# Kernel tuning notes

Hardware: AMD Instinct MI355X
Metric: run time of the kernel (lower is better)

The kernel has to match this reference:

```python
import jax, jax.numpy as jnp
import numpy as np

FEAT_DIM = 128

def conv3(x, w, b):
    y = jax.lax.conv_general_dilated(x, w, (1, 1), 'SAME', dimension_numbers=('NCHW', 'OIHW', 'NCHW'))
    return y + b[None, :, None, None]

def edsr(x, hw, hb, rw, rb, tw, tb):
    # EDSR baseline encoder (no upsampling): head conv, n resblocks, tail conv, global skip
    x = conv3(x, hw, hb)
    res = x
    for i in range(rw.shape[0]):
        t = jax.nn.relu(conv3(res, rw[i, 0], rb[i, 0]))
        res = res + conv3(t, rw[i, 1], rb[i, 1])
    return conv3(res, tw, tb) + x

def maxpool(x, k):
    return jax.lax.reduce_window(x, -jnp.inf, jax.lax.max, (1, 1, k, k), (1, 1, k, k), 'VALID')

def make_coord(h, w):
    ys = -1.0 + (2.0 * jnp.arange(h, dtype=jnp.float32) + 1.0) / h
    xs = -1.0 + (2.0 * jnp.arange(w, dtype=jnp.float32) + 1.0) / w
    yy, xx = jnp.meshgrid(ys, xs, indexing='ij')
    return jnp.stack([yy, xx], axis=-1)  # [h,w,2] (y,x)

def sample_nearest(img, coord):
    # F.grid_sample nearest, align_corners=False, zeros padding.
    # img [b,c,hi,wi]; coord [b,N,2] normalized (y,x) -> [b,N,c]
    b, c, hi, wi = img.shape
    iy = jnp.round(((coord[..., 0] + 1.0) * hi - 1.0) / 2.0)
    ix = jnp.round(((coord[..., 1] + 1.0) * wi - 1.0) / 2.0)
    valid = (iy >= 0) & (iy < hi) & (ix >= 0) & (ix < wi)
    idx = (jnp.clip(iy, 0, hi - 1) * wi + jnp.clip(ix, 0, wi - 1)).astype(jnp.int32)
    out = jnp.take_along_axis(img.reshape(b, c, hi * wi), idx[:, None, :], axis=2)
    out = jnp.where(valid[:, None, :], out, jnp.zeros((), img.dtype))
    return out.transpose(0, 2, 1)

def mlp2(x, w1, b1, w2, b2):
    return jax.nn.gelu(x @ w1 + b1, approximate=False) @ w2 + b2

def level(feat, coord, hr_guide, hr_guide_lr, im_w, im_b, wg, ffn, residual):
    b, c, h, w = feat.shape
    Hh, Ww = hr_guide.shape[2], hr_guide.shape[3]
    N = coord.shape[0]
    coord = jnp.broadcast_to(coord[None], (b, N, 2))
    fc = jnp.broadcast_to(make_coord(h, w).transpose(2, 0, 1)[None], (b, 2, h, w))
    g_s = sample_nearest(hr_guide, coord)  # [b,N,guide_dim]
    scale = jnp.array([h, w], dtype=jnp.float32)
    preds = []
    for vx in (-1.0, 1.0):
        for vy in (-1.0, 1.0):
            coord_ = coord + jnp.array([vx / h, vy / w], dtype=jnp.float32)
            f_s = sample_nearest(feat, coord_)
            gl_s = sample_nearest(hr_guide_lr, coord_)
            c_s = sample_nearest(fc, coord_)
            rel = (coord - c_s) * scale
            inp = jnp.concatenate([f_s, g_s, gl_s, rel], axis=-1)  # [b,N,3*fd+2]
            pred = jax.nn.relu(inp @ im_w + im_b)  # MLP(hidden_list=None): Linear+ReLU
            preds.append(pred[..., :FEAT_DIM])
            preds.append(pred[..., FEAT_DIM:])
    preds = jnp.stack(preds, axis=-2)  # [b,N,8,fd]
    weight = jax.nn.softmax(mlp2(preds, *wg), axis=-2)
    recon = jnp.sum(preds * weight, axis=-2)  # [b,N,fd]
    out = mlp2(recon, *ffn)
    if residual:
        out = out + recon
    return out.transpose(0, 2, 1).reshape(b, -1, Hh, Ww)

def setup_inputs():
    ks = jax.random.split(jax.random.key(0), 24)
    fd, nb, nsb = 128, 31, 3
    B, H, W, hlr = 16, 64, 64, 16
    def w_(k, shape, fan):
        return jax.random.normal(k, shape, dtype=jnp.float32) * (fan ** -0.5)
    return {
        'HR_MSI': jax.random.normal(ks[0], (B, nsb, H, W), dtype=jnp.float32),
        'lms': jax.random.normal(ks[1], (B, nb, H, W), dtype=jnp.float32),
        'LR_HSI': jax.random.normal(ks[2], (B, nb, hlr, hlr), dtype=jnp.float32),
        'spa_head_w': w_(ks[3], (fd, nsb + nb, 3, 3), (nsb + nb) * 9), 'spa_head_b': jnp.zeros((fd,)),
        'spa_res_w': w_(ks[4], (4, 2, fd, fd, 3, 3), fd * 9), 'spa_res_b': jnp.zeros((4, 2, fd)),
        'spa_tail_w': w_(ks[5], (fd, fd, 3, 3), fd * 9), 'spa_tail_b': jnp.zeros((fd,)),
        'spe_head_w': w_(ks[6], (fd, nb, 3, 3), nb * 9), 'spe_head_b': jnp.zeros((fd,)),
        'spe_res_w': w_(ks[7], (4, 2, fd, fd, 3, 3), fd * 9), 'spe_res_b': jnp.zeros((4, 2, fd)),
        'spe_tail_w': w_(ks[8], (fd, fd, 3, 3), fd * 9), 'spe_tail_b': jnp.zeros((fd,)),
        'l1_w': w_(ks[9], (fd * 3 + 2, fd * 2), fd * 3 + 2), 'l1_b': jnp.zeros((fd * 2,)),
        'wg32_w1': w_(ks[10], (fd, 64), fd), 'wg32_b1': jnp.zeros((64,)),
        'wg32_w2': w_(ks[11], (64, fd), 64), 'wg32_b2': jnp.zeros((fd,)),
        'ffn32_w1': w_(ks[12], (fd, 64), fd), 'ffn32_b1': jnp.zeros((64,)),
        'ffn32_w2': w_(ks[13], (64, fd), 64), 'ffn32_b2': jnp.zeros((fd,)),
        'l2_w': w_(ks[14], (fd * 3 + 2, fd * 2), fd * 3 + 2), 'l2_b': jnp.zeros((fd * 2,)),
        'wg64_w1': w_(ks[15], (fd, 64), fd), 'wg64_b1': jnp.zeros((64,)),
        'wg64_w2': w_(ks[16], (64, fd), 64), 'wg64_b2': jnp.zeros((fd,)),
        'ffn64_w1': w_(ks[17], (fd, 64), fd), 'ffn64_b1': jnp.zeros((64,)),
        'ffn64_w2': w_(ks[18], (64, nb), 64), 'ffn64_b2': jnp.zeros((nb,)),
    }

def reference(HR_MSI, lms, LR_HSI, spa_head_w, spa_head_b, spa_res_w, spa_res_b, spa_tail_w, spa_tail_b, spe_head_w, spe_head_b, spe_res_w, spe_res_b, spe_tail_w, spe_tail_b, l1_w, l1_b, wg32_w1, wg32_b1, wg32_w2, wg32_b2, ffn32_w1, ffn32_b1, ffn32_w2, ffn32_b2, l2_w, l2_b, wg64_w1, wg64_b1, wg64_w2, wg64_b2, ffn64_w1, ffn64_b1, ffn64_w2, ffn64_b2):
    b, _, H, W = HR_MSI.shape
    hr_spa = edsr(jnp.concatenate([HR_MSI, lms], axis=1), spa_head_w, spa_head_b, spa_res_w, spa_res_b, spa_tail_w, spa_tail_b)
    guide32 = maxpool(hr_spa, H // 32)   # AdaptiveMaxPool2d -> 32x32
    guide16 = maxpool(hr_spa, H // 16)   # AdaptiveMaxPool2d -> 16x16
    lr_spe = edsr(LR_HSI, spe_head_w, spe_head_b, spe_res_w, spe_res_b, spe_tail_w, spe_tail_b)
    coord32 = make_coord(H // 2, W // 2).reshape(-1, 2)
    coord64 = make_coord(H, W).reshape(-1, 2)
    l1 = level(lr_spe, coord32, guide32, guide16, l1_w, l1_b, (wg32_w1, wg32_b1, wg32_w2, wg32_b2), (ffn32_w1, ffn32_b1, ffn32_w2, ffn32_b2), True)
    l2 = level(l1, coord64, hr_spa, guide32, l2_w, l2_b, (wg64_w1, wg64_b1, wg64_w2, wg64_b2), (ffn64_w1, ffn64_b1, ffn64_w2, ffn64_b2), False)
    return lms + l2
```

## Files before the change

### kernel.cpp

```cpp
#include <hip/hip_runtime.h>
#include <math.h>

typedef _Float16 f16;
typedef __attribute__((ext_vector_type(4))) _Float16 f16x4;
typedef __attribute__((ext_vector_type(8))) _Float16 f16x8;
typedef __attribute__((ext_vector_type(4))) float f32x4;
typedef __attribute__((ext_vector_type(4))) unsigned int u32x4;

__device__ __forceinline__ float gelu_f(float x) {
    float xs = x * 0.70710678118654752440f;
    float ax = fabsf(xs);
    float t = __builtin_amdgcn_rcpf(1.0f + 0.3275911f * ax);
    float p = t * (0.254829592f + t * (-0.284496736f + t * (1.421413741f +
              t * (-1.453152027f + t * 1.061405429f))));
    float erfv = 1.0f - p * __expf(-ax * ax);
    erfv = copysignf(erfv, xs);
    return 0.5f * x * (1.0f + erfv);
}

__device__ __forceinline__ void nsamp(float cy, float cx, int hi, int wi,
                                      int& iy, int& ix, bool& valid) {
    float fy = rintf(((cy + 1.0f) * (float)hi - 1.0f) * 0.5f);
    float fx = rintf(((cx + 1.0f) * (float)wi - 1.0f) * 0.5f);
    valid = (fy >= 0.0f) && (fy < (float)hi) && (fx >= 0.0f) && (fx < (float)wi);
    iy = (int)fminf(fmaxf(fy, 0.0f), (float)(hi - 1));
    ix = (int)fminf(fmaxf(fx, 0.0f), (float)(wi - 1));
}

__global__ __launch_bounds__(256) void pack_w(
    const float* __restrict__ src, f16* __restrict__ dst,
    int Cin, int NCHUNK, int total) {
    int i = blockIdx.x * 256 + threadIdx.x;
    if (i >= total) return;
    int ci = i & 31;
    int tap = (i >> 5) % 9;
    int q = i / 288;
    int chunk = q % NCHUNK;
    int q2 = q / NCHUNK;
    int cout = q2 & 127;
    int conv = q2 >> 7;
    int cin = chunk * 32 + ci;
    float v = (cin < Cin) ? src[((size_t)(conv * 128 + cout) * Cin + cin) * 9 + tap] : 0.f;
    dst[i] = (f16)v;
}

__global__ __launch_bounds__(256) void pack_lvl(
    const float* __restrict__ src, f16* __restrict__ dst,
    int Ksrc, int N, int NC) {
    int i = blockIdx.x * 256 + threadIdx.x;
    if (i >= N * NC * 32) return;
    int kk = i & 31;
    int c = (i >> 5) % NC;
    int n = i / (32 * NC);
    int k = c * 32 + kk;
    dst[i] = (f16)((k < Ksrc) ? src[(size_t)k * N + n] : 0.f);
}

__global__ __launch_bounds__(256) void build_cc(
    const float* __restrict__ msi, const float* __restrict__ lms,
    f16* __restrict__ out, int total) {
    int i = blockIdx.x * 256 + threadIdx.x;
    if (i >= total) return;
    int ch = i % 34;
    int p = i / 34;
    int x = p & 63, y = (p >> 6) & 63, b = p >> 12;
    float v = (ch < 3) ? msi[(((size_t)(b * 3 + ch) << 6) + y << 6) + x]
                       : lms[(((size_t)(b * 31 + ch - 3) << 6) + y << 6) + x];
    out[((size_t)(b * 66 + y + 1) * 66 + x + 1) * 64 + ch] = v;
}

__global__ __launch_bounds__(256) void build_spe(
    const float* __restrict__ in, f16* __restrict__ out, int total) {
    int i = blockIdx.x * 256 + threadIdx.x;
    if (i >= total) return;
    int ch = i % 31;
    int p = i / 31;
    int x = p & 15, y = (p >> 4) & 15, b = p >> 8;
    out[((size_t)(b * 18 + y + 1) * 18 + x + 1) * 32 + ch] =
        (f16)in[(((size_t)(b * 31 + ch) << 4) + y << 4) + x];
}

template<int PXW, int XSH, int ROWS, int WAVES>
__global__ __launch_bounds__(WAVES * 64) void conv_mfma(
    const f16* __restrict__ in_h, int NCHUNK,
    const f16* __restrict__ wp, const float* __restrict__ bias,
    const f16* __restrict__ skip_h, f16* __restrict__ out_h,
    f16* __restrict__ out2, int mode) {
    constexpr int XW = 1 << XSH;
    constexpr int PH = XW + 2;
    constexpr int NPX = (ROWS + 2) * PXW;
    constexpr int UNITS = NPX * 4;
    constexpr int NTH = WAVES * 64;
    constexpr int ITER = (UNITS + NTH - 1) / NTH;
    constexpr int WN = WAVES / 2;
    constexpr int NT = 8 / WN;
    constexpr int MT = (ROWS << XSH) >> 5;
    __shared__ u32x4 ldsv[UNITS];
    char* ldsb = (char*)ldsv;

    int tid = threadIdx.x;
    constexpr int NYB = XW / ROWS;
    int b = blockIdx.x / NYB;
    int y0 = (blockIdx.x % NYB) * ROWS;
    int wave = tid >> 6, lane = tid & 63;
    int wm = wave / WN, wn = wave % WN;
    int l15 = lane & 15, lk = lane >> 4;
    int CST = NCHUNK * 32;

    int gaddr[ITER], laddr[ITER];
#pragma unroll
    for (int i = 0; i < ITER; ++i) {
        int u = tid + NTH * i;
        if (u < UNITS) {
            int px = u >> 2, kg = u & 3;
            int r = px / PXW, xp = px - r * PXW;
            gaddr[i] = ((b * PH + y0 + r) * PXW + xp) * CST + kg * 8;
            laddr[i] = (u * 16) ^ (((px >> 1) & 3) << 4);
        } else {
            gaddr[i] = -1; laddr[i] = 0;
        }
    }

    f32x4 acc[MT][NT];
#pragma unroll
    for (int mt = 0; mt < MT; ++mt)
#pragma unroll
        for (int nt = 0; nt < NT; ++nt)
            acc[mt][nt] = (f32x4){0.f, 0.f, 0.f, 0.f};

    u32x4 v[ITER];
#pragma unroll
    for (int i = 0; i < ITER; ++i)
        if (gaddr[i] >= 0) v[i] = *(const u32x4*)(in_h + gaddr[i]);

    for (int c = 0; c < NCHUNK; ++c) {
        if (c) __syncthreads();
#pragma unroll
        for (int i = 0; i < ITER; ++i)
            if (gaddr[i] >= 0) *(u32x4*)(ldsb + laddr[i]) = v[i];
        __syncthreads();
        if (c + 1 < NCHUNK) {
#pragma unroll
            for (int i = 0; i < ITER; ++i)
                if (gaddr[i] >= 0) v[i] = *(const u32x4*)(in_h + gaddr[i] + (c + 1) * 32);
        }
#pragma unroll
        for (int tap = 0; tap < 9; ++tap) {
            const int dy = tap / 3, dx = tap % 3;
            f16x8 afr[MT];
#pragma unroll
            for (int mt = 0; mt < MT; ++mt) {
                int px = (wm * MT + mt) * 16 + l15;
                int row = px >> XSH, x = px & (XW - 1);
                int pxl = (row + dy) * PXW + x + dx;
                int la = pxl * 64 + lk * 16;
                afr[mt] = *(const f16x8*)(ldsb + (la ^ (((pxl >> 1) & 3) << 4)));
            }
#pragma unroll
            for (int nt = 0; nt < NT; ++nt) {
                int cout = wn * (NT * 16) + nt * 16 + l15;
                f16x8 bfr = *(const f16x8*)(wp + ((size_t)(cout * NCHUNK + c) * 9 + tap) * 32 + lk * 8);
#pragma unroll
                for (int mt = 0; mt < MT; ++mt)
                    acc[mt][nt] = __builtin_amdgcn_mfma_f32_16x16x32_f16(afr[mt], bfr, acc[mt][nt], 0, 0, 0);
            }
        }
    }

#pragma unroll
    for (int mt = 0; mt < MT; ++mt)
#pragma unroll
        for (int nt = 0; nt < NT; ++nt) {
            int cout = wn * (NT * 16) + nt * 16 + l15;
            float bv = bias[cout];
#pragma unroll
            for (int reg = 0; reg < 4; ++reg) {
                int px = (wm * MT + mt) * 16 + lk * 4 + reg;
                int row = px >> XSH, x = px & (XW - 1);
                int yim = y0 + row;
                float vv = acc[mt][nt][reg] + bv;
                size_t ah = ((size_t)(b * PH + yim + 1) * PXW + x + 1) * 128 + cout;
                if (mode == 1) vv = fmaxf(vv, 0.f);
                if (mode == 2) vv += (float)out_h[ah];
                if (mode == 3) {
                    vv += (float)skip_h[ah];
                    out2[((size_t)((b << XSH) + yim) << XSH | x) * 128 + cout] = (f16)vv;
                } else if (mode == 4) {
                    f16 hv = (f16)vv;
                    out_h[ah] = hv;
                    out2[ah] = hv;
                } else {
                    out_h[ah] = (f16)vv;
                }
            }
        }
}

__global__ __launch_bounds__(256) void maxpool_nhwc(
    const f16* __restrict__ in, f16* __restrict__ out,
    int H, int W, int k, int total) {
    int i = blockIdx.x * 256 + threadIdx.x;
    if (i >= total) return;
    int c = i & 127;
    int r = i >> 7;
    int Wo = W / k, Ho = H / k;
    int x = r % Wo; r /= Wo;
    int y = r % Ho;
    int b = r / Ho;
    float m = -3.402823466e38f;
    for (int dy = 0; dy < k; ++dy)
        for (int dx = 0; dx < k; ++dx)
            m = fmaxf(m, (float)in[((size_t)(b * H + y * k + dy) * W + x * k + dx) * 128 + c]);
    out[i] = (f16)m;
}

__global__ __launch_bounds__(256) void level_kernel(
    const f16* __restrict__ featT, int fh, int fw,
    const f16* __restrict__ guideT, int Hg, int Wg,
    const f16* __restrict__ glrT, int hl, int wl,
    int Hq, int Wq, int n_per_b,
    const f16* __restrict__ imw_h, const float* __restrict__ imb,
    const f16* __restrict__ w1h, const float* __restrict__ b1,
    const f16* __restrict__ w2h, const float* __restrict__ b2,
    const f16* __restrict__ f1h, const float* __restrict__ fb1,
    const f16* __restrict__ f2h, const float* __restrict__ fb2,
    int odim, int residual, int out_nchw,
    const float* __restrict__ lms,
    f16* __restrict__ out16, float* __restrict__ outf) {
    __shared__ char smem[58624];
    f16* s_inp  = (f16*)smem;
    f16* s_pred = (f16*)smem;
    f16* s_h1   = (f16*)(smem + 34816);
    f16* s_hh   = (f16*)smem;
    f16* s_rec  = (f16*)(smem + 54272);

    int tid = threadIdx.x;
    int b = blockIdx.x / n_per_b;
    int n0 = (blockIdx.x % n_per_b) * 16;
    float invHq = 1.0f / (float)Hq, invWq = 1.0f / (float)Wq;
    float invfh = 1.0f / (float)fh, invfw = 1.0f / (float)fw;
    int wave = tid >> 6, lane = tid & 63;
    int l15 = lane & 15, lk = lane >> 4;

    {
        const int r64 = tid >> 2, t4 = tid & 3;
        const int cidx = r64 >> 4, q = r64 & 15;
        int n = n0 + q;
        int qy = n / Wq, qx = n - qy * Wq;
        float cy = -1.0f + (float)(2 * qy + 1) * invHq;
        float cx = -1.0f + (float)(2 * qx + 1) * invWq;
        float vxc = (cidx < 2) ? -1.0f : 1.0f;
        float vyc = (cidx & 1) ? 1.0f : -1.0f;
        float cy_ = cy + vxc * invfh;
        float cx_ = cx + vyc * invfw;
        int iy, ix; bool vf;
        nsamp(cy_, cx_, fh, fw, iy, ix, vf);
        const f16* fp = featT + ((size_t)(b * fh + iy) * fw + ix) * 128;
        int gy, gx; bool vg0;
        nsamp(cy, cx, Hg, Wg, gy, gx, vg0);
        const f16* gp = guideT + ((size_t)(b * Hg + gy) * Wg + gx) * 128;
        int ly, lx; bool vl;
        nsamp(cy_, cx_, hl, wl, ly, lx, vl);
        const f16* lp = glrT + ((size_t)(b * hl + ly) * wl + lx) * 128;
        f16* row = s_inp + r64 * 424;
        const u32x4 zz = (u32x4){0, 0, 0, 0};
#pragma unroll
        for (int e = 0; e < 4; ++e) {
            int d0 = t4 * 8 + e * 32;
            u32x4 av = vf ? *(const u32x4*)(fp + d0) : zz;
            u32x4 gv = vg0 ? *(const u32x4*)(gp + d0) : zz;
            u32x4 lv = vl ? *(const u32x4*)(lp + d0) : zz;
            *(u32x4*)(row + d0) = av;
            *(u32x4*)(row + 128 + d0) = gv;
            *(u32x4*)(row + 256 + d0) = lv;
        }
        if (t4 == 0) {
#pragma unroll
            for (int e = 0; e < 4; ++e)
                *(u32x4*)((char*)row + 768 + e * 16) = zz;
            float csy = vf ? (-1.0f + (float)(2 * iy + 1) * invfh) : 0.0f;
            float csx = vf ? (-1.0f + (float)(2 * ix + 1) * invfw) : 0.0f;
            row[384] = (f16)((cy - csy) * (float)fh);
            row[385] = (f16)((cx - csx) * (float)fw);
        }
    }
    __syncthreads();

    f32x4 acc[4][4];
    {
#pragma unroll
        for (int mt = 0; mt < 4; ++mt)
#pragma unroll
            for (int nt = 0; nt < 4; ++nt)
                acc[mt][nt] = (f32x4){0.f, 0.f, 0.f, 0.f};
        int nbase = wave * 64;
#pragma unroll
        for (int ks = 0; ks < 13; ++ks) {
            f16x8 afr[4];
#pragma unroll
            for (int mt = 0; mt < 4; ++mt)
                afr[mt] = *(const f16x8*)((char*)s_inp + (mt * 16 + l15) * 848 + ks * 64 + lk * 16);
#pragma unroll
            for (int nt = 0; nt < 4; ++nt) {
                f16x8 bfr = *(const f16x8*)(imw_h + ((size_t)(nbase + nt * 16 + l15) * 13 + ks) * 32 + lk * 8);
#pragma unroll
                for (int mt = 0; mt < 4; ++mt)
                    acc[mt][nt] = __builtin_amdgcn_mfma_f32_16x16x32_f16(afr[mt], bfr, acc[mt][nt], 0, 0, 0);
            }
        }
    }
    __syncthreads();

    {
        int nbase = wave * 64;
#pragma unroll
        for (int nt = 0; nt < 4; ++nt) {
            int col = nbase + nt * 16 + l15;
            float bv = imb[col];
            int j_hi = col >> 7, d = col & 127;
#pragma unroll
            for (int mt = 0; mt < 4; ++mt)
#pragma unroll
                for (int reg = 0; reg < 4; ++reg) {
                    int row64 = mt * 16 + lk * 4 + reg;
                    int q = row64 & 15, cidx = row64 >> 4;
                    int qj = q * 8 + cidx * 2 + j_hi;
                    s_pred[qj * 136 + d] = (f16)fmaxf(acc[mt][nt][reg] + bv, 0.f);
                }
        }
    }
    __syncthreads();

    {
        f32x4 a1[8];
#pragma unroll
        for (int mt = 0; mt < 8; ++mt) a1[mt] = (f32x4){0.f, 0.f, 0.f, 0.f};
        int c1 = wave * 16 + l15;
#pragma unroll
        for (int ks = 0; ks < 4; ++ks) {
            f16x8 bfr = *(const f16x8*)(w1h + ((size_t)c1 * 4 + ks) * 32 + lk * 8);
#pragma unroll
            for (int mt = 0; mt < 8; ++mt) {
                f16x8 afr = *(const f16x8*)((char*)s_pred + (mt * 16 + l15) * 272 + ks * 64 + lk * 16);
                a1[mt] = __builtin_amdgcn_mfma_f32_16x16x32_f16(afr, bfr, a1[mt], 0, 0, 0);
            }
        }
        float bb1 = b1[c1];
#pragma unroll
        for (int mt = 0; mt < 8; ++mt)
#pragma unroll
            for (int reg = 0; reg < 4; ++reg) {
                int row = mt * 16 + lk * 4 + reg;
                s_h1[row * 72 + c1] = (f16)gelu_f(a1[mt][reg] + bb1);
            }
    }
    __syncthreads();

    {
        f32x4 a2[8][2];
#pragma unroll
        for (int mt = 0; mt < 8; ++mt) {
            a2[mt][0] = (f32x4){0.f, 0.f, 0.f, 0.f};
            a2[mt][1] = (f32x4){0.f, 0.f, 0.f, 0.f};
        }
#pragma unroll
        for (int ks = 0; ks < 2; ++ks) {
#pragma unroll
            for (int nt = 0; nt < 2; ++nt) {
                int c2 = wave * 32 + nt * 16 + l15;
                f16x8 bfr = *(const f16x8*)(w2h + ((size_t)c2 * 2 + ks) * 32 + lk * 8);
#pragma unroll
                for (int mt = 0; mt < 8; ++mt) {
                    f16x8 afr = *(const f16x8*)((char*)s_h1 + (mt * 16 + l15) * 144 + ks * 64 + lk * 16);
                    a2[mt][nt] = __builtin_amdgcn_mfma_f32_16x16x32_f16(afr, bfr, a2[mt][nt], 0, 0, 0);
                }
            }
        }
        int qhalf = lk >> 1;
#pragma unroll
        for (int nt = 0; nt < 2; ++nt) {
            int col = wave * 32 + nt * 16 + l15;
            float bb2 = b2[col];
#pragma unroll
            for (int mt = 0; mt < 8; ++mt) {
                int q = mt * 2 + qhalf;
                float v[4];
                float mloc = -3.4e38f;
#pragma unroll
                for (int reg = 0; reg < 4; ++reg) {
                    v[reg] = a2[mt][nt][reg] + bb2;
                    mloc = fmaxf(mloc, v[reg]);
                }
                float mf = fmaxf(mloc, __shfl_xor(mloc, 16));
                float e[4], sl = 0.f;
#pragma unroll
                for (int reg = 0; reg < 4; ++reg) {
                    e[reg] = __expf(v[reg] - mf);
                    sl += e[reg];
                }
                float sf = sl + __shfl_xor(sl, 16);
                float inv = 1.0f / sf;
                float rp = 0.f;
#pragma unroll
                for (int reg = 0; reg < 4; ++reg) {
                    int row = mt * 16 + lk * 4 + reg;
                    rp += (float)s_pred[row * 136 + col] * e[reg];
                }
                rp *= inv;
                float rf = rp + __shfl_xor(rp, 16);
                if ((lk & 1) == 0) s_rec[q * 136 + col] = (f16)rf;
            }
        }
    }
    __syncthreads();

    {
        f32x4 a1 = (f32x4){0.f, 0.f, 0.f, 0.f};
        int c1 = wave * 16 + l15;
#pragma unroll
        for (int ks = 0; ks < 4; ++ks) {
            f16x8 afr = *(const f16x8*)((char*)s_rec + l15 * 272 + ks * 64 + lk * 16);
            f16x8 bfr = *(const f16x8*)(f1h + ((size_t)c1 * 4 + ks) * 32 + lk * 8);
            a1 = __builtin_amdgcn_mfma_f32_16x16x32_f16(afr, bfr, a1, 0, 0, 0);
        }
        float bb = fb1[c1];
#pragma unroll
        for (int reg = 0; reg < 4; ++reg) {
            int row = lk * 4 + reg;
            s_hh[row * 72 + c1] = (f16)gelu_f(a1[reg] + bb);
        }
    }
    __syncthreads();

    if (!out_nchw) {
        f32x4 a2[2];
        a2[0] = (f32x4){0.f, 0.f, 0.f, 0.f};
        a2[1] = (f32x4){0.f, 0.f, 0.f, 0.f};
#pragma unroll
        for (int ks = 0; ks < 2; ++ks) {
            f16x8 afr = *(const f16x8*)((char*)s_hh + l15 * 144 + ks * 64 + lk * 16);
#pragma unroll
            for (int nt = 0; nt < 2; ++nt) {
                int col = wave * 32 + nt * 16 + l15;
                f16x8 bfr = *(const f16x8*)(f2h + ((size_t)col * 2 + ks) * 32 + lk * 8);
                a2[nt] = __builtin_amdgcn_mfma_f32_16x16x32_f16(afr, bfr, a2[nt], 0, 0, 0);
            }
        }
#pragma unroll
        for (int nt = 0; nt < 2; ++nt) {
            int col = wave * 32 + nt * 16 + l15;
            float bb = fb2[col];
#pragma unroll
            for (int reg = 0; reg < 4; ++reg) {
                int q = lk * 4 + reg;
                int n = n0 + q;
                int qy = n / Wq, qx = n - qy * Wq;
                float val = a2[nt][reg] + bb;
                if (residual) val += (float)s_rec[q * 136 + col];
                out16[((size_t)(b * Hq + qy) * Wq + qx) * 128 + col] = (f16)val;
            }
        }
    } else {
        if (wave < 2) {
            f32x4 a2 = (f32x4){0.f, 0.f, 0.f, 0.f};
#pragma unroll
            for (int ks = 0; ks < 2; ++ks) {
                f16x8 afr = *(const f16x8*)((char*)s_hh + l15 * 144 + ks * 64 + lk * 16);
                int col = wave * 16 + l15;
                f16x8 bfr = *(const f16x8*)(f2h + ((size_t)col * 2 + ks) * 32 + lk * 8);
                a2 = __builtin_amdgcn_mfma_f32_16x16x32_f16(afr, bfr, a2, 0, 0, 0);
            }
            int d = wave * 16 + l15;
            if (d < odim) {
                float bb = fb2[d];
#pragma unroll
                for (int reg = 0; reg < 4; ++reg) {
                    int q = lk * 4 + reg;
                    int n = n0 + q;
                    int qy = n / Wq, qx = n - qy * Wq;
                    size_t oi = (((size_t)b * odim + d) * Hq + qy) * Wq + qx;
                    outf[oi] = a2[reg] + bb + lms[oi];
                }
            }
        }
    }
}

#define WPACK_B   0ull
#define CC_B      5529600ull
#define SPEIN_B   (CC_B)
#define X2_B      (CC_B + 331776ull)
#define R2_B      (CC_B + 1658880ull)
#define T2_B      (CC_B + 2985984ull)
#define RH_B      14450688ull
#define TH_B      32292864ull
#define XH_B      50135040ull
#define G32_B     (TH_B)
#define G16_B     (TH_B + 4194304ull)
#define L1T_B     (TH_B + 5242880ull)
#define LRSPE_B   (CC_B + 4313088ull)
#define HR16_B    67977216ull
#define LVLW_B    101531648ull
#define L1IMW_B   (LVLW_B)
#define L1W1_B    (LVLW_B + 212992ull)
#define L1W2_B    (LVLW_B + 229376ull)
#define L1F1_B    (LVLW_B + 245760ull)
#define L1F2_B    (LVLW_B + 262144ull)
#define L2IMW_B   (LVLW_B + 278528ull)
#define L2W1_B    (LVLW_B + 491520ull)
#define L2W2_B    (LVLW_B + 507904ull)
#define L2F1_B    (LVLW_B + 524288ull)
#define L2F2_B    (LVLW_B + 540672ull)

extern "C" void kernel_launch(void* const* d_in, const int* in_sizes, int n_in,
                              void* d_out, int out_size, void* d_ws, size_t ws_size,
                              hipStream_t stream) {
    (void)in_sizes; (void)n_in; (void)out_size; (void)ws_size;
    const float* HR_MSI     = (const float*)d_in[0];
    const float* lms        = (const float*)d_in[1];
    const float* LR_HSI     = (const float*)d_in[2];
    const float* spa_head_w = (const float*)d_in[3];
    const float* spa_head_b = (const float*)d_in[4];
    const float* spa_res_w  = (const float*)d_in[5];
    const float* spa_res_b  = (const float*)d_in[6];
    const float* spa_tail_w = (const float*)d_in[7];
    const float* spa_tail_b = (const float*)d_in[8];
    const float* spe_head_w = (const float*)d_in[9];
    const float* spe_head_b = (const float*)d_in[10];
    const float* spe_res_w  = (const float*)d_in[11];
    const float* spe_res_b  = (const float*)d_in[12];
    const float* spe_tail_w = (const float*)d_in[13];
    const float* spe_tail_b = (const float*)d_in[14];
    const float* l1_w   = (const float*)d_in[15];
    const float* l1_b   = (const float*)d_in[16];
    const float* wg32_w1 = (const float*)d_in[17];
    const float* wg32_b1 = (const float*)d_in[18];
    const float* wg32_w2 = (const float*)d_in[19];
    const float* wg32_b2 = (const float*)d_in[20];
    const float* ffn32_w1 = (const float*)d_in[21];
    const float* ffn32_b1 = (const float*)d_in[22];
    const float* ffn32_w2 = (const float*)d_in[23];
    const float* ffn32_b2 = (const float*)d_in[24];
    const float* l2_w   = (const float*)d_in[25];
    const float* l2_b   = (const float*)d_in[26];
    const float* wg64_w1 = (const float*)d_in[27];
    const float* wg64_b1 = (const float*)d_in[28];
    const float* wg64_w2 = (const float*)d_in[29];
    const float* wg64_b2 = (const float*)d_in[30];
    const float* ffn64_w1 = (const float*)d_in[31];
    const float* ffn64_b1 = (const float*)d_in[32];
    const float* ffn64_w2 = (const float*)d_in[33];
    const float* ffn64_b2 = (const float*)d_in[34];

    char* ws = (char*)d_ws;
    f16* Wp      = (f16*)(ws + WPACK_B);
    f16* Cc      = (f16*)(ws + CC_B);
    f16* SPEin   = (f16*)(ws + SPEIN_B);
    f16* X2h     = (f16*)(ws + X2_B);
    f16* R2h     = (f16*)(ws + R2_B);
    f16* T2h     = (f16*)(ws + T2_B);
    f16* lrspe16 = (f16*)(ws + LRSPE_B);
    f16* Rh      = (f16*)(ws + RH_B);
    f16* Xh      = (f16*)(ws + XH_B);
    f16* Th      = (f16*)(ws + TH_B);
    f16* g32T    = (f16*)(ws + G32_B);
    f16* g16T    = (f16*)(ws + G16_B);
    f16* l1T16   = (f16*)(ws + L1T_B);
    f16* hr16    = (f16*)(ws + HR16_B);
    f16* l1imw = (f16*)(ws + L1IMW_B);
    f16* l1w1  = (f16*)(ws + L1W1_B);
    f16* l1w2  = (f16*)(ws + L1W2_B);
    f16* l1f1  = (f16*)(ws + L1F1_B);
    f16* l1f2  = (f16*)(ws + L1F2_B);
    f16* l2imw = (f16*)(ws + L2IMW_B);
    f16* l2w1  = (f16*)(ws + L2W1_B);
    f16* l2w2  = (f16*)(ws + L2W2_B);
    f16* l2f1  = (f16*)(ws + L2F1_B);
    f16* l2f2  = (f16*)(ws + L2F2_B);

    hipMemsetAsync(ws + CC_B, 0, 8921088ull, stream);
    hipMemsetAsync(ws + RH_B, 0, 53526528ull, stream);

    pack_w<<<288, 256, 0, stream>>>(spa_head_w, Wp + 0, 34, 2, 73728);
    pack_w<<<4608, 256, 0, stream>>>(spa_res_w, Wp + 73728, 128, 4, 1179648);
    pack_w<<<576, 256, 0, stream>>>(spa_tail_w, Wp + 1253376, 128, 4, 147456);
    pack_w<<<144, 256, 0, stream>>>(spe_head_w, Wp + 1400832, 31, 1, 36864);
    pack_w<<<4608, 256, 0, stream>>>(spe_res_w, Wp + 1437696, 128, 4, 1179648);
    pack_w<<<576, 256, 0, stream>>>(spe_tail_w, Wp + 2617344, 128, 4, 147456);

    pack_lvl<<<416, 256, 0, stream>>>(l1_w, l1imw, 386, 256, 13);
    pack_lvl<<<32, 256, 0, stream>>>(wg32_w1, l1w1, 128, 64, 4);
    pack_lvl<<<32, 256, 0, stream>>>(wg32_w2, l1w2, 64, 128, 2);
    pack_lvl<<<32, 256, 0, stream>>>(ffn32_w1, l1f1, 128, 64, 4);
    pack_lvl<<<32, 256, 0, stream>>>(ffn32_w2, l1f2, 64, 128, 2);
    pack_lvl<<<416, 256, 0, stream>>>(l2_w, l2imw, 386, 256, 13);
    pack_lvl<<<32, 256, 0, stream>>>(wg64_w1, l2w1, 128, 64, 4);
    pack_lvl<<<32, 256, 0, stream>>>(wg64_w2, l2w2, 64, 128, 2);
    pack_lvl<<<32, 256, 0, stream>>>(ffn64_w1, l2f1, 128, 64, 4);
    pack_lvl<<<8, 256, 0, stream>>>(ffn64_w2, l2f2, 64, 31, 2);

    build_cc<<<8704, 256, 0, stream>>>(HR_MSI, lms, Cc, 16 * 64 * 64 * 34);
    conv_mfma<66, 6, 2, 8><<<512, 512, 0, stream>>>(Cc, 2, Wp + 0, spa_head_b,
                                                    nullptr, Xh, Rh, 4);
    hipMemsetAsync(ws + SPEIN_B, 0, 5361664ull, stream);
    for (int i = 0; i < 4; ++i) {
        conv_mfma<66, 6, 2, 8><<<512, 512, 0, stream>>>(
            Rh, 4, Wp + 73728 + (size_t)(2 * i) * 147456, spa_res_b + 2 * i * 128,
            nullptr, Th, nullptr, 1);
        conv_mfma<66, 6, 2, 8><<<512, 512, 0, stream>>>(
            Th, 4, Wp + 73728 + (size_t)(2 * i + 1) * 147456, spa_res_b + (2 * i + 1) * 128,
            nullptr, Rh, nullptr, 2);
    }
    conv_mfma<66, 6, 2, 8><<<512, 512, 0, stream>>>(Rh, 4, Wp + 1253376, spa_tail_b,
                                                    Xh, nullptr, hr16, 3);

    maxpool_nhwc<<<8192, 256, 0, stream>>>(hr16, g32T, 64, 64, 2, 2097152);
    maxpool_nhwc<<<2048, 256, 0, stream>>>(hr16, g16T, 64, 64, 4, 524288);

    build_spe<<<496, 256, 0, stream>>>(LR_HSI, SPEin, 16 * 16 * 16 * 31);
    conv_mfma<18, 4, 4, 4><<<64, 256, 0, stream>>>(SPEin, 1, Wp + 1400832, spe_head_b,
                                                   nullptr, X2h, R2h, 4);
    for (int i = 0; i < 4; ++i) {
        conv_mfma<18, 4, 4, 4><<<64, 256, 0, stream>>>(
            R2h, 4, Wp + 1437696 + (size_t)(2 * i) * 147456, spe_res_b + 2 * i * 128,
            nullptr, T2h, nullptr, 1);
        conv_mfma<18, 4, 4, 4><<<64, 256, 0, stream>>>(
            T2h, 4, Wp + 1437696 + (size_t)(2 * i + 1) * 147456, spe_res_b + (2 * i + 1) * 128,
            nullptr, R2h, nullptr, 2);
    }
    conv_mfma<18, 4, 4, 4><<<64, 256, 0, stream>>>(R2h, 4, Wp + 2617344, spe_tail_b,
                                                   X2h, nullptr, lrspe16, 3);

    level_kernel<<<1024, 256, 0, stream>>>(
        lrspe16, 16, 16, g32T, 32, 32, g16T, 16, 16,
        32, 32, 64,
        l1imw, l1_b, l1w1, wg32_b1, l1w2, wg32_b2,
        l1f1, ffn32_b1, l1f2, ffn32_b2,
        128, 1, 0, nullptr, l1T16, nullptr);

    level_kernel<<<4096, 256, 0, stream>>>(
        l1T16, 32, 32, hr16, 64, 64, g32T, 32, 32,
        64, 64, 256,
        l2imw, l2_b, l2w1, wg64_b1, l2w2, wg64_b2,
        l2f1, ffn64_b1, l2f2, ffn64_b2,
        31, 0, 1, lms, nullptr, (float*)d_out);
}
```

Before: 1.039 ms.

## Stage full input-channel tile in LDS once per conv block

The conv kernel now loads the whole halo tile across all input-channel chunks into LDS in one pass with a single barrier, replacing the per-chunk register-prefetch loop with its two barriers per chunk. NCHUNK becomes a template parameter so the chunk loop fully unrolls, and the swizzle is widened to 8 positions. The small spectral convs switch from 4 rows per block to 2, doubling the grid to 128 blocks for better CU coverage. In exchange, LDS per block grows up to 4x (about 67 KB for the 64x64 convs), which may limit occupancy despite the added launch-bounds hint, and there is no longer any overlap between global loads and MFMA work within a block.

Measured after the change: 1.027 ms. Within noise of the previous version (-1.1%).

```diff
diff --git a/kernel.cpp b/kernel.cpp
--- a/kernel.cpp
+++ b/kernel.cpp
@@ -80,23 +80,24 @@
         (f16)in[(((size_t)(b * 31 + ch) << 4) + y << 4) + x];
 }
 
-template<int PXW, int XSH, int ROWS, int WAVES>
-__global__ __launch_bounds__(WAVES * 64) void conv_mfma(
-    const f16* __restrict__ in_h, int NCHUNK,
+template<int PXW, int XSH, int ROWS, int WAVES, int NCHUNK>
+__global__ __launch_bounds__(WAVES * 64, 4) void conv_mfma(
+    const f16* __restrict__ in_h,
     const f16* __restrict__ wp, const float* __restrict__ bias,
     const f16* __restrict__ skip_h, f16* __restrict__ out_h,
     f16* __restrict__ out2, int mode) {
     constexpr int XW = 1 << XSH;
     constexpr int PH = XW + 2;
     constexpr int NPX = (ROWS + 2) * PXW;
-    constexpr int UNITS = NPX * 4;
+    constexpr int UPP = NCHUNK * 4;
+    constexpr int UNITS = NPX * UPP;
     constexpr int NTH = WAVES * 64;
     constexpr int ITER = (UNITS + NTH - 1) / NTH;
     constexpr int WN = WAVES / 2;
     constexpr int NT = 8 / WN;
     constexpr int MT = (ROWS << XSH) >> 5;
-    __shared__ u32x4 ldsv[UNITS];
-    char* ldsb = (char*)ldsv;
+    constexpr int PXB = NCHUNK * 64;
+    __shared__ char ldsb[NPX * PXB];
 
     int tid = threadIdx.x;
     constexpr int NYB = XW / ROWS;
@@ -105,21 +106,19 @@
     int wave = tid >> 6, lane = tid & 63;
     int wm = wave / WN, wn = wave % WN;
     int l15 = lane & 15, lk = lane >> 4;
-    int CST = NCHUNK * 32;
-
-    int gaddr[ITER], laddr[ITER];
+
 #pragma unroll
     for (int i = 0; i < ITER; ++i) {
         int u = tid + NTH * i;
         if (u < UNITS) {
-            int px = u >> 2, kg = u & 3;
+            int px = u / UPP, kg = u % UPP;
             int r = px / PXW, xp = px - r * PXW;
-            gaddr[i] = ((b * PH + y0 + r) * PXW + xp) * CST + kg * 8;
-            laddr[i] = (u * 16) ^ (((px >> 1) & 3) << 4);
-        } else {
-            gaddr[i] = -1; laddr[i] = 0;
-        }
-    }
+            u32x4 v = *(const u32x4*)(in_h +
+                (size_t)((b * PH + y0 + r) * PXW + xp) * (NCHUNK * 32) + kg * 8);
+            *(u32x4*)(ldsb + ((u * 16) ^ ((px & 7) << 4))) = v;
+        }
+    }
+    __syncthreads();
 
     f32x4 acc[MT][NT];
 #pragma unroll
@@ -128,22 +127,8 @@
         for (int nt = 0; nt < NT; ++nt)
             acc[mt][nt] = (f32x4){0.f, 0.f, 0.f, 0.f};
 
-    u32x4 v[ITER];
-#pragma unroll
-    for (int i = 0; i < ITER; ++i)
-        if (gaddr[i] >= 0) v[i] = *(const u32x4*)(in_h + gaddr[i]);
-
+#pragma unroll
     for (int c = 0; c < NCHUNK; ++c) {
-        if (c) __syncthreads();
-#pragma unroll
-        for (int i = 0; i < ITER; ++i)
-            if (gaddr[i] >= 0) *(u32x4*)(ldsb + laddr[i]) = v[i];
-        __syncthreads();
-        if (c + 1 < NCHUNK) {
-#pragma unroll
-            for (int i = 0; i < ITER; ++i)
-                if (gaddr[i] >= 0) v[i] = *(const u32x4*)(in_h + gaddr[i] + (c + 1) * 32);
-        }
 #pragma unroll
         for (int tap = 0; tap < 9; ++tap) {
             const int dy = tap / 3, dx = tap % 3;
@@ -153,8 +138,8 @@
                 int px = (wm * MT + mt) * 16 + l15;
                 int row = px >> XSH, x = px & (XW - 1);
                 int pxl = (row + dy) * PXW + x + dx;
-                int la = pxl * 64 + lk * 16;
-                afr[mt] = *(const f16x8*)(ldsb + (la ^ (((pxl >> 1) & 3) << 4)));
+                int la = pxl * PXB + c * 64 + lk * 16;
+                afr[mt] = *(const f16x8*)(ldsb + (la ^ ((pxl & 7) << 4)));
             }
 #pragma unroll
             for (int nt = 0; nt < NT; ++nt) {
@@ -600,36 +585,36 @@
     pack_lvl<<<8, 256, 0, stream>>>(ffn64_w2, l2f2, 64, 31, 2);
 
     build_cc<<<8704, 256, 0, stream>>>(HR_MSI, lms, Cc, 16 * 64 * 64 * 34);
-    conv_mfma<66, 6, 2, 8><<<512, 512, 0, stream>>>(Cc, 2, Wp + 0, spa_head_b,
-                                                    nullptr, Xh, Rh, 4);
+    conv_mfma<66, 6, 2, 8, 2><<<512, 512, 0, stream>>>(Cc, Wp + 0, spa_head_b,
+                                                       nullptr, Xh, Rh, 4);
     hipMemsetAsync(ws + SPEIN_B, 0, 5361664ull, stream);
     for (int i = 0; i < 4; ++i) {
-        conv_mfma<66, 6, 2, 8><<<512, 512, 0, stream>>>(
-            Rh, 4, Wp + 73728 + (size_t)(2 * i) * 147456, spa_res_b + 2 * i * 128,
+        conv_mfma<66, 6, 2, 8, 4><<<512, 512, 0, stream>>>(
+            Rh, Wp + 73728 + (size_t)(2 * i) * 147456, spa_res_b + 2 * i * 128,
             nullptr, Th, nullptr, 1);
-        conv_mfma<66, 6, 2, 8><<<512, 512, 0, stream>>>(
-            Th, 4, Wp + 73728 + (size_t)(2 * i + 1) * 147456, spa_res_b + (2 * i + 1) * 128,
+        conv_mfma<66, 6, 2, 8, 4><<<512, 512, 0, stream>>>(
+            Th, Wp + 73728 + (size_t)(2 * i + 1) * 147456, spa_res_b + (2 * i + 1) * 128,
             nullptr, Rh, nullptr, 2);
     }
-    conv_mfma<66, 6, 2, 8><<<512, 512, 0, stream>>>(Rh, 4, Wp + 1253376, spa_tail_b,
-                                                    Xh, nullptr, hr16, 3);
+    conv_mfma<66, 6, 2, 8, 4><<<512, 512, 0, stream>>>(Rh, Wp + 1253376, spa_tail_b,
+                                                       Xh, nullptr, hr16, 3);
 
     maxpool_nhwc<<<8192, 256, 0, stream>>>(hr16, g32T, 64, 64, 2, 2097152);
     maxpool_nhwc<<<2048, 256, 0, stream>>>(hr16, g16T, 64, 64, 4, 524288);
 
     build_spe<<<496, 256, 0, stream>>>(LR_HSI, SPEin, 16 * 16 * 16 * 31);
-    conv_mfma<18, 4, 4, 4><<<64, 256, 0, stream>>>(SPEin, 1, Wp + 1400832, spe_head_b,
-                                                   nullptr, X2h, R2h, 4);
+    conv_mfma<18, 4, 2, 4, 1><<<128, 256, 0, stream>>>(SPEin, Wp + 1400832, spe_head_b,
+                                                       nullptr, X2h, R2h, 4);
     for (int i = 0; i < 4; ++i) {
-        conv_mfma<18, 4, 4, 4><<<64, 256, 0, stream>>>(
-            R2h, 4, Wp + 1437696 + (size_t)(2 * i) * 147456, spe_res_b + 2 * i * 128,
+        conv_mfma<18, 4, 2, 4, 4><<<128, 256, 0, stream>>>(
+            R2h, Wp + 1437696 + (size_t)(2 * i) * 147456, spe_res_b + 2 * i * 128,
             nullptr, T2h, nullptr, 1);
-        conv_mfma<18, 4, 4, 4><<<64, 256, 0, stream>>>(
-            T2h, 4, Wp + 1437696 + (size_t)(2 * i + 1) * 147456, spe_res_b + (2 * i + 1) * 128,
+        conv_mfma<18, 4, 2, 4, 4><<<128, 256, 0, stream>>>(
+            T2h, Wp + 1437696 + (size_t)(2 * i + 1) * 147456, spe_res_b + (2 * i + 1) * 128,
             nullptr, R2h, nullptr, 2);
     }
-    conv_mfma<18, 4, 4, 4><<<64, 256, 0, stream>>>(R2h, 4, Wp + 2617344, spe_tail_b,
-                                                   X2h, nullptr, lrspe16, 3);
+    conv_mfma<18, 4, 2, 4, 4><<<128, 256, 0, stream>>>(R2h, Wp + 2617344, spe_tail_b,
+                                                       X2h, nullptr, lrspe16, 3);
 
     level_kernel<<<1024, 256, 0, stream>>>(
         lrspe16, 16, 16, g32T, 32, 32, g16T, 16, 16,
```
